# Optimization experiments

Hardware: AMD Instinct MI355X
Metric: run time of the kernel (lower is better)

Reference implementation:

```python
import jax, jax.numpy as jnp
import numpy as np

R = 32
LORA_ALPHA = 64
SCALING = LORA_ALPHA / R  # 2.0
TOPK = 2
NOISE_EPS = 0.01


def setup_inputs() -> dict:
    key = jax.random.key(0)
    ks = jax.random.split(key, 7)
    B, S, D, OUT, E = 4, 2048, 4096, 4096, 8
    x = jax.random.normal(ks[0], (B, S, D), dtype=jnp.float32)
    eof_index = jax.random.randint(ks[1], (B,), 0, S)
    noise = jax.random.normal(ks[2], (B, E), dtype=jnp.float32)
    # learned params (random instead of the zero-init in reset_parameters so the
    # output is non-trivial); Linear weight layout is [out_features, in_features]
    A_w = jax.random.normal(ks[3], (R, D), dtype=jnp.float32) * (1.0 / np.sqrt(D))
    B_w = jax.random.normal(ks[4], (E, OUT, R), dtype=jnp.float32) * (1.0 / np.sqrt(R))
    route_w = jax.random.normal(ks[5], (E, D), dtype=jnp.float32) * (1.0 / np.sqrt(D))
    noise_w = jax.random.normal(ks[6], (E, D), dtype=jnp.float32) * (1.0 / np.sqrt(D))
    return {"x": x, "eof_index": eof_index, "noise": noise,
            "A_w": A_w, "B_w": B_w, "route_w": route_w, "noise_w": noise_w}


def reference(x, eof_index, noise, A_w, B_w, route_w, noise_w):
    B = x.shape[0]
    rows = jnp.arange(B)
    # routing input: token at eof_index for each batch row -> [B, D]
    routing_input = x[rows, eof_index]
    # noisy top-k gating (training path: noisy_gating and is_train are True)
    clean_logits = routing_input @ route_w.T                       # [B, E]
    noise_stddev = jax.nn.softplus(routing_input @ noise_w.T) + NOISE_EPS
    logits = clean_logits + noise * noise_stddev                   # [B, E]
    # torch code takes topk+1 then slices to topk; equivalent to top_k(topk)
    top_vals, top_idx = jax.lax.top_k(logits, TOPK)                # [B, K]
    top_gates = jax.nn.softmax(top_vals.astype(jnp.float32), axis=-1).astype(x.dtype)
    gates = jnp.zeros_like(logits).at[rows[:, None], top_idx].set(top_gates)  # [B, E]
    # shared low-rank projection
    shared = jnp.einsum('bsd,rd->bsr', x, A_w)                     # [B, S, r]
    # sum_i gate_i * (shared @ B_i^T), fused as one contraction
    lora_output = jnp.einsum('bsr,eor,be->bso', shared, B_w, gates)  # [B, S, out]
    return lora_output * SCALING
```

## Files before the change

### kernel.cpp

```cpp
#include <hip/hip_runtime.h>
#include <stdint.h>
#include <math.h>

#define B_ 4
#define S_ 2048
#define D_ 4096
#define O_ 4096
#define E_ 8
#define R_ 32
#define SCALING 2.0f
#define NOISE_EPS 0.01f

typedef unsigned short u16;
typedef short s16x8 __attribute__((ext_vector_type(8)));
typedef float f32x4 __attribute__((ext_vector_type(4)));

__device__ __forceinline__ float b2f(u16 u) {
  union { unsigned int i; float f; } v; v.i = ((unsigned int)u) << 16; return v.f;
}
__device__ __forceinline__ u16 f2b(float f) {
  union { unsigned int i; float f; } v; v.f = f;
  unsigned int i = v.i;
  return (u16)((i + 0x7FFFu + ((i >> 16) & 1u)) >> 16);
}
__device__ __forceinline__ void split2(float f, u16* h, u16* l) {
  u16 hi = f2b(f);
  *h = hi;
  *l = f2b(f - b2f(hi));
}

__device__ __forceinline__ float ld(const void* p, size_t i, int bf) {
  return bf ? b2f(((const u16*)p)[i]) : ((const float*)p)[i];
}

__global__ void k_detect(const unsigned int* __restrict__ xw, int* __restrict__ flag) {
  __shared__ int cnt;
  if (threadIdx.x == 0) cnt = 0;
  __syncthreads();
  unsigned int w = xw[threadIdx.x];
  unsigned int e = (w >> 7) & 0xFFu;
  if (e >= 90u && e <= 140u) atomicAdd(&cnt, 1);
  __syncthreads();
  if (threadIdx.x == 0) *flag = (cnt > 48) ? 1 : 0;
}

__global__ __launch_bounds__(256) void k_logits(
    const void* __restrict__ x, const int* __restrict__ eof,
    const void* __restrict__ route_w, const void* __restrict__ noise_w,
    const int* __restrict__ flag, float* __restrict__ wsf) {
  int bf = *flag;
  int be = blockIdx.x;
  int b = be >> 3, e = be & 7;
  size_t xoff = ((size_t)b * S_ + (size_t)eof[b]) * D_;
  size_t woff = (size_t)e * D_;
  float ac = 0.f, an = 0.f;
  for (int d = threadIdx.x; d < D_; d += 256) {
    float xv = ld(x, xoff + d, bf);
    ac += xv * ld(route_w, woff + d, bf);
    an += xv * ld(noise_w, woff + d, bf);
  }
  __shared__ float rc[256], rn[256];
  rc[threadIdx.x] = ac; rn[threadIdx.x] = an;
  __syncthreads();
  for (int s = 128; s > 0; s >>= 1) {
    if (threadIdx.x < (unsigned)s) {
      rc[threadIdx.x] += rc[threadIdx.x + s];
      rn[threadIdx.x] += rn[threadIdx.x + s];
    }
    __syncthreads();
  }
  if (threadIdx.x == 0) { wsf[16 + be] = rc[0]; wsf[48 + be] = rn[0]; }
}

__global__ void k_gates(const void* __restrict__ noise, const int* __restrict__ flag,
                        float* __restrict__ wsf) {
  int bf = *flag;
  int b = threadIdx.x;
  if (b >= B_) return;
  float lg[E_];
  for (int e = 0; e < E_; e++) {
    float c = wsf[16 + b * 8 + e];
    float n = wsf[48 + b * 8 + e];
    float sp = (n > 20.f) ? n : log1pf(expf(n));
    lg[e] = c + ld(noise, b * 8 + e, bf) * (sp + NOISE_EPS);
  }
  int i1 = 0; float v1 = lg[0];
  for (int e = 1; e < E_; e++) if (lg[e] > v1) { v1 = lg[e]; i1 = e; }
  int i2 = -1; float v2 = -3.0e38f;
  for (int e = 0; e < E_; e++) if (e != i1 && lg[e] > v2) { v2 = lg[e]; i2 = e; }
  float t = expf(v2 - v1);
  float g1 = 1.f / (1.f + t);
  float g2 = t / (1.f + t);
  for (int e = 0; e < E_; e++) wsf[80 + b * 8 + e] = 0.f;
  wsf[80 + b * 8 + i1] = g1;
  wsf[80 + b * 8 + i2] = g2;
}

__global__ __launch_bounds__(256) void k_prepA(
    const float* __restrict__ Aw, const int* __restrict__ flag,
    u16* __restrict__ Aph, u16* __restrict__ Apl) {
  if (*flag) return;
  int flat = blockIdx.x * 256 + threadIdx.x;
  int k32idx = flat >> 7;
  int rem = flat & 127;
  int h = rem >> 6;
  int lane = rem & 63;
  int r = h * 16 + (lane & 15);
  int d = k32idx * 32 + (lane >> 4) * 8;
  const float* src = Aw + (size_t)r * D_ + d;
  f32x4 v0 = *(const f32x4*)src;
  f32x4 v1 = *(const f32x4*)(src + 4);
  ushort4 h0, l0, h1, l1;
  split2(v0[0], &h0.x, &l0.x); split2(v0[1], &h0.y, &l0.y);
  split2(v0[2], &h0.z, &l0.z); split2(v0[3], &h0.w, &l0.w);
  split2(v1[0], &h1.x, &l1.x); split2(v1[1], &h1.y, &l1.y);
  split2(v1[2], &h1.z, &l1.z); split2(v1[3], &h1.w, &l1.w);
  *(ushort4*)(Aph + (size_t)flat * 8)     = h0;
  *(ushort4*)(Aph + (size_t)flat * 8 + 4) = h1;
  *(ushort4*)(Apl + (size_t)flat * 8)     = l0;
  *(ushort4*)(Apl + (size_t)flat * 8 + 4) = l1;
}

__global__ __launch_bounds__(256) void k_wc(
    const void* __restrict__ Bw, const int* __restrict__ flag,
    const float* __restrict__ gates, u16* __restrict__ Wph,
    u16* __restrict__ Wpl) {
  int bf = *flag;
  int idx = blockIdx.x * 256 + threadIdx.x;
  int b = idx >> 15;
  int u = idx & 32767;
  int o = u >> 3, rq = u & 7;
  float g[E_];
#pragma unroll
  for (int e = 0; e < E_; e++) g[e] = gates[b * 8 + e];
  f32x4 acc = {0.f, 0.f, 0.f, 0.f};
  if (bf) {
#pragma unroll
    for (int e = 0; e < E_; e++) {
      ushort4 v = ((const ushort4*)Bw)[(size_t)e * 32768 + u];
      acc[0] += g[e] * b2f(v.x);
      acc[1] += g[e] * b2f(v.y);
      acc[2] += g[e] * b2f(v.z);
      acc[3] += g[e] * b2f(v.w);
    }
  } else {
#pragma unroll
    for (int e = 0; e < E_; e++) {
      f32x4 v = ((const f32x4*)Bw)[(size_t)e * 32768 + u];
      acc += g[e] * v;
    }
  }
  acc *= SCALING;
  ushort4 h, l;
  split2(acc[0], &h.x, &l.x); split2(acc[1], &h.y, &l.y);
  split2(acc[2], &h.z, &l.z); split2(acc[3], &h.w, &l.w);
  int ot = o >> 4;
  int lane = ((rq >> 1) * 16) + (o & 15);
  size_t base = (((size_t)b * 256 + ot) * 64 + lane) * 8 + (rq & 1) * 4;
  *(ushort4*)(Wph + base) = h;
  *(ushort4*)(Wpl + base) = l;
}

__global__ __launch_bounds__(256) void k_sharedM(
    const void* __restrict__ xv, const void* __restrict__ Awv,
    const u16* __restrict__ Aph, const u16* __restrict__ Apl,
    const int* __restrict__ flag, u16* __restrict__ sh2h,
    u16* __restrict__ sh2l) {
  __shared__ u16 xh[4096];
  __shared__ u16 xl[4096];
  __shared__ float red[4][512];
  int bf = *flag;
  int t = threadIdx.x;
  int lane = t & 63;
  int wave = t >> 6;
  int m = lane & 15, kg = lane >> 4;
  int row0 = blockIdx.x * 16;
  f32x4 acc0 = {0.f, 0.f, 0.f, 0.f};
  f32x4 acc1 = {0.f, 0.f, 0.f, 0.f};
  if (bf) {
    int kbase = wave * 1024 + kg * 8;
    const u16* xp = (const u16*)xv + (size_t)(row0 + m) * D_ + kbase;
    const u16* a0 = (const u16*)Awv + (size_t)m * D_ + kbase;
    const u16* a1 = (const u16*)Awv + (size_t)(m + 16) * D_ + kbase;
#pragma unroll 4
    for (int k0 = 0; k0 < 1024; k0 += 32) {
      s16x8 a  = *(const s16x8*)(xp + k0);
      s16x8 b0 = *(const s16x8*)(a0 + k0);
      s16x8 b1 = *(const s16x8*)(a1 + k0);
      acc0 = __builtin_amdgcn_mfma_f32_16x16x32_bf16(a, b0, acc0, 0, 0, 0);
      acc1 = __builtin_amdgcn_mfma_f32_16x16x32_bf16(a, b1, acc1, 0, 0, 0);
    }
  } else {
    int srow = t >> 4;
    int sq = t & 15;
    const float* xrow = (const float*)xv + (size_t)(row0 + srow) * D_;
    for (int kc = 0; kc < D_; kc += 256) {
      __syncthreads();
#pragma unroll
      for (int q = 0; q < 4; q++) {
        int colf = (sq + q * 16) * 4;
        f32x4 v = *(const f32x4*)(xrow + kc + colf);
        ushort4 h, l;
        split2(v[0], &h.x, &l.x); split2(v[1], &h.y, &l.y);
        split2(v[2], &h.z, &l.z); split2(v[3], &h.w, &l.w);
        int swz = (srow * 512 + colf * 2) ^ ((srow & 7) << 4);
        *(ushort4*)((char*)xh + swz) = h;
        *(ushort4*)((char*)xl + swz) = l;
      }
      __syncthreads();
#pragma unroll
      for (int p = 0; p < 2; p++) {
        int k32 = (wave * 2 + p) * 32;
        int boff = (m * 512 + (k32 + kg * 8) * 2) ^ ((m & 7) << 4);
        s16x8 ah = *(const s16x8*)((const char*)xh + boff);
        s16x8 al = *(const s16x8*)((const char*)xl + boff);
        size_t k32idx = (size_t)(kc >> 5) + wave * 2 + p;
        const u16* ph = Aph + (k32idx * 2) * 512;
        const u16* pl = Apl + (k32idx * 2) * 512;
        s16x8 bh0 = *(const s16x8*)(ph + (size_t)lane * 8);
        s16x8 bl0 = *(const s16x8*)(pl + (size_t)lane * 8);
        s16x8 bh1 = *(const s16x8*)(ph + 512 + (size_t)lane * 8);
        s16x8 bl1 = *(const s16x8*)(pl + 512 + (size_t)lane * 8);
        acc0 = __builtin_amdgcn_mfma_f32_16x16x32_bf16(ah, bh0, acc0, 0, 0, 0);
        acc0 = __builtin_amdgcn_mfma_f32_16x16x32_bf16(ah, bl0, acc0, 0, 0, 0);
        acc0 = __builtin_amdgcn_mfma_f32_16x16x32_bf16(al, bh0, acc0, 0, 0, 0);
        acc1 = __builtin_amdgcn_mfma_f32_16x16x32_bf16(ah, bh1, acc1, 0, 0, 0);
        acc1 = __builtin_amdgcn_mfma_f32_16x16x32_bf16(ah, bl1, acc1, 0, 0, 0);
        acc1 = __builtin_amdgcn_mfma_f32_16x16x32_bf16(al, bh1, acc1, 0, 0, 0);
      }
    }
    __syncthreads();
  }
  int crow = (lane >> 4) * 4, ccol = lane & 15;
#pragma unroll
  for (int j = 0; j < 4; j++) {
    red[wave][(crow + j) * 32 + ccol]      = acc0[j];
    red[wave][(crow + j) * 32 + ccol + 16] = acc1[j];
  }
  __syncthreads();
#pragma unroll
  for (int q = 0; q < 2; q++) {
    int e = t + q * 256;
    float s = red[0][e] + red[1][e] + red[2][e] + red[3][e];
    u16 h, l;
    split2(s, &h, &l);
    int row = e >> 5, r = e & 31;
    size_t dst = (size_t)blockIdx.x * 512 + ((size_t)(r >> 3) * 16 + row) * 8 + (r & 7);
    sh2h[dst] = h;
    sh2l[dst] = l;
  }
}

#define OCH 512
__global__ __launch_bounds__(256) void k_outM(
    const u16* __restrict__ sh2h, const u16* __restrict__ sh2l,
    const u16* __restrict__ Wph, const u16* __restrict__ Wpl,
    const int* __restrict__ flag, void* __restrict__ out) {
  __shared__ float C[16][516];
  int bf = *flag;
  int t = threadIdx.x;
  int lane = t & 63, wave = t >> 6;
  int row0 = blockIdx.x * 16;
  int b = row0 >> 11;
  int m = lane & 15;
  s16x8 Ah = *(const s16x8*)(sh2h + (size_t)blockIdx.x * 512 + (size_t)lane * 8);
  s16x8 Al = *(const s16x8*)(sh2l + (size_t)blockIdx.x * 512 + (size_t)lane * 8);
  int crow = (lane >> 4) * 4;
  const u16* whB = Wph + (size_t)b * 131072;
  const u16* wlB = Wpl + (size_t)b * 131072;
  for (int oc = 0; oc < O_; oc += OCH) {
#pragma unroll
    for (int i = 0; i < 8; i++) {
      int otc = wave * 8 + i;
      size_t otg = (size_t)((oc >> 4) + otc);
      s16x8 Bh = *(const s16x8*)(whB + otg * 512 + (size_t)lane * 8);
      s16x8 Bl = *(const s16x8*)(wlB + otg * 512 + (size_t)lane * 8);
      f32x4 acc = {0.f, 0.f, 0.f, 0.f};
      acc = __builtin_amdgcn_mfma_f32_16x16x32_bf16(Ah, Bh, acc, 0, 0, 0);
      acc = __builtin_amdgcn_mfma_f32_16x16x32_bf16(Ah, Bl, acc, 0, 0, 0);
      acc = __builtin_amdgcn_mfma_f32_16x16x32_bf16(Al, Bh, acc, 0, 0, 0);
      int ocol = otc * 16 + m;
#pragma unroll
      for (int j = 0; j < 4; j++) C[crow + j][ocol] = acc[j];
    }
    __syncthreads();
#pragma unroll
    for (int it = 0; it < 8; it++) {
      int row = it * 2 + (t >> 7);
      int col = (t & 127) * 4;
      f32x4 v = *(const f32x4*)&C[row][col];
      size_t off = (size_t)(row0 + row) * O_ + oc + col;
      if (bf) {
        ushort4 o4;
        o4.x = f2b(v[0]); o4.y = f2b(v[1]); o4.z = f2b(v[2]); o4.w = f2b(v[3]);
        *(ushort4*)((u16*)out + off) = o4;
      } else {
        *(f32x4*)((float*)out + off) = v;
      }
    }
    __syncthreads();
  }
}

extern "C" void kernel_launch(void* const* d_in, const int* in_sizes, int n_in,
                              void* d_out, int out_size, void* d_ws, size_t ws_size,
                              hipStream_t stream) {
  const void* x       = d_in[0];
  const int*  eof     = (const int*)d_in[1];
  const void* noise   = d_in[2];
  const void* Aw      = d_in[3];
  const void* Bw      = d_in[4];
  const void* route_w = d_in[5];
  const void* noise_w = d_in[6];
  float* wsf = (float*)d_ws;
  int* flag = (int*)wsf;
  float* gates = wsf + 80;
  u16* Wph  = (u16*)(wsf + 112);
  u16* Wpl  = Wph + (size_t)B_ * O_ * R_;
  u16* Aph  = Wpl + (size_t)B_ * O_ * R_;
  u16* Apl  = Aph + (size_t)R_ * D_;
  u16* sh2h = Apl + (size_t)R_ * D_;
  u16* sh2l = sh2h + (size_t)B_ * S_ * R_;

  k_detect<<<1, 64, 0, stream>>>((const unsigned int*)x, flag);
  k_logits<<<B_ * E_, 256, 0, stream>>>(x, eof, route_w, noise_w, flag, wsf);
  k_gates<<<1, 64, 0, stream>>>(noise, flag, wsf);
  k_prepA<<<64, 256, 0, stream>>>((const float*)Aw, flag, Aph, Apl);
  k_wc<<<(B_ * O_ * R_ / 4) / 256, 256, 0, stream>>>(Bw, flag, gates, Wph, Wpl);
  k_sharedM<<<(B_ * S_) / 16, 256, 0, stream>>>(x, Aw, Aph, Apl, flag, sh2h, sh2l);
  k_outM<<<(B_ * S_) / 16, 256, 0, stream>>>(sh2h, sh2l, Wph, Wpl, flag, d_out);
}
```

Baseline: 315.1 us.

## Fuse shared projection and output GEMM into one kernel, merge prep kernels

Merges the A-weight split and the gated B-weight combine into a single prep launch that picks its role by block index. Fuses the shared low-rank projection and the output GEMM into one kernel: the 16x32 intermediate stays in LDS instead of going to global memory, and the x staging buffer and output staging buffer share a union. This removes two launches and a global round trip for the intermediate, at the cost of higher LDS use per block and a larger fused kernel that may lower occupancy.

```diff
diff --git a/kernel.cpp b/kernel.cpp
--- a/kernel.cpp
+++ b/kernel.cpp
@@ -96,85 +96,90 @@
   wsf[80 + b * 8 + i2] = g2;
 }
 
-__global__ __launch_bounds__(256) void k_prepA(
-    const float* __restrict__ Aw, const int* __restrict__ flag,
+__global__ __launch_bounds__(256) void k_prep(
+    const void* __restrict__ Bw, const float* __restrict__ Aw,
+    const int* __restrict__ flag, const float* __restrict__ gates,
+    u16* __restrict__ Wph, u16* __restrict__ Wpl,
     u16* __restrict__ Aph, u16* __restrict__ Apl) {
-  if (*flag) return;
-  int flat = blockIdx.x * 256 + threadIdx.x;
-  int k32idx = flat >> 7;
-  int rem = flat & 127;
-  int h = rem >> 6;
-  int lane = rem & 63;
-  int r = h * 16 + (lane & 15);
-  int d = k32idx * 32 + (lane >> 4) * 8;
-  const float* src = Aw + (size_t)r * D_ + d;
-  f32x4 v0 = *(const f32x4*)src;
-  f32x4 v1 = *(const f32x4*)(src + 4);
-  ushort4 h0, l0, h1, l1;
-  split2(v0[0], &h0.x, &l0.x); split2(v0[1], &h0.y, &l0.y);
-  split2(v0[2], &h0.z, &l0.z); split2(v0[3], &h0.w, &l0.w);
-  split2(v1[0], &h1.x, &l1.x); split2(v1[1], &h1.y, &l1.y);
-  split2(v1[2], &h1.z, &l1.z); split2(v1[3], &h1.w, &l1.w);
-  *(ushort4*)(Aph + (size_t)flat * 8)     = h0;
-  *(ushort4*)(Aph + (size_t)flat * 8 + 4) = h1;
-  *(ushort4*)(Apl + (size_t)flat * 8)     = l0;
-  *(ushort4*)(Apl + (size_t)flat * 8 + 4) = l1;
-}
-
-__global__ __launch_bounds__(256) void k_wc(
-    const void* __restrict__ Bw, const int* __restrict__ flag,
-    const float* __restrict__ gates, u16* __restrict__ Wph,
-    u16* __restrict__ Wpl) {
   int bf = *flag;
-  int idx = blockIdx.x * 256 + threadIdx.x;
-  int b = idx >> 15;
-  int u = idx & 32767;
-  int o = u >> 3, rq = u & 7;
-  float g[E_];
-#pragma unroll
-  for (int e = 0; e < E_; e++) g[e] = gates[b * 8 + e];
-  f32x4 acc = {0.f, 0.f, 0.f, 0.f};
-  if (bf) {
-#pragma unroll
-    for (int e = 0; e < E_; e++) {
-      ushort4 v = ((const ushort4*)Bw)[(size_t)e * 32768 + u];
-      acc[0] += g[e] * b2f(v.x);
-      acc[1] += g[e] * b2f(v.y);
-      acc[2] += g[e] * b2f(v.z);
-      acc[3] += g[e] * b2f(v.w);
-    }
+  int blk = blockIdx.x;
+  if (blk < 512) {
+    int idx = blk * 256 + threadIdx.x;
+    int b = idx >> 15;
+    int u = idx & 32767;
+    int o = u >> 3, rq = u & 7;
+    float g[E_];
+#pragma unroll
+    for (int e = 0; e < E_; e++) g[e] = gates[b * 8 + e];
+    f32x4 acc = {0.f, 0.f, 0.f, 0.f};
+    if (bf) {
+#pragma unroll
+      for (int e = 0; e < E_; e++) {
+        ushort4 v = ((const ushort4*)Bw)[(size_t)e * 32768 + u];
+        acc[0] += g[e] * b2f(v.x);
+        acc[1] += g[e] * b2f(v.y);
+        acc[2] += g[e] * b2f(v.z);
+        acc[3] += g[e] * b2f(v.w);
+      }
+    } else {
+#pragma unroll
+      for (int e = 0; e < E_; e++) {
+        f32x4 v = ((const f32x4*)Bw)[(size_t)e * 32768 + u];
+        acc += g[e] * v;
+      }
+    }
+    acc *= SCALING;
+    ushort4 h, l;
+    split2(acc[0], &h.x, &l.x); split2(acc[1], &h.y, &l.y);
+    split2(acc[2], &h.z, &l.z); split2(acc[3], &h.w, &l.w);
+    int ot = o >> 4;
+    int lane = ((rq >> 1) * 16) + (o & 15);
+    size_t base = (((size_t)b * 256 + ot) * 64 + lane) * 8 + (rq & 1) * 4;
+    *(ushort4*)(Wph + base) = h;
+    *(ushort4*)(Wpl + base) = l;
   } else {
-#pragma unroll
-    for (int e = 0; e < E_; e++) {
-      f32x4 v = ((const f32x4*)Bw)[(size_t)e * 32768 + u];
-      acc += g[e] * v;
-    }
-  }
-  acc *= SCALING;
-  ushort4 h, l;
-  split2(acc[0], &h.x, &l.x); split2(acc[1], &h.y, &l.y);
-  split2(acc[2], &h.z, &l.z); split2(acc[3], &h.w, &l.w);
-  int ot = o >> 4;
-  int lane = ((rq >> 1) * 16) + (o & 15);
-  size_t base = (((size_t)b * 256 + ot) * 64 + lane) * 8 + (rq & 1) * 4;
-  *(ushort4*)(Wph + base) = h;
-  *(ushort4*)(Wpl + base) = l;
-}
-
-__global__ __launch_bounds__(256) void k_sharedM(
+    if (bf) return;
+    int flat = (blk - 512) * 256 + threadIdx.x;
+    int k32idx = flat >> 7;
+    int rem = flat & 127;
+    int hf = rem >> 6;
+    int lane = rem & 63;
+    int r = hf * 16 + (lane & 15);
+    int d = k32idx * 32 + (lane >> 4) * 8;
+    const float* src = Aw + (size_t)r * D_ + d;
+    f32x4 v0 = *(const f32x4*)src;
+    f32x4 v1 = *(const f32x4*)(src + 4);
+    ushort4 h0, l0, h1, l1;
+    split2(v0[0], &h0.x, &l0.x); split2(v0[1], &h0.y, &l0.y);
+    split2(v0[2], &h0.z, &l0.z); split2(v0[3], &h0.w, &l0.w);
+    split2(v1[0], &h1.x, &l1.x); split2(v1[1], &h1.y, &l1.y);
+    split2(v1[2], &h1.z, &l1.z); split2(v1[3], &h1.w, &l1.w);
+    *(ushort4*)(Aph + (size_t)flat * 8)     = h0;
+    *(ushort4*)(Aph + (size_t)flat * 8 + 4) = h1;
+    *(ushort4*)(Apl + (size_t)flat * 8)     = l0;
+    *(ushort4*)(Apl + (size_t)flat * 8 + 4) = l1;
+  }
+}
+
+#define OCH 512
+__global__ __launch_bounds__(256) void k_mega(
     const void* __restrict__ xv, const void* __restrict__ Awv,
     const u16* __restrict__ Aph, const u16* __restrict__ Apl,
-    const int* __restrict__ flag, u16* __restrict__ sh2h,
-    u16* __restrict__ sh2l) {
-  __shared__ u16 xh[4096];
-  __shared__ u16 xl[4096];
-  __shared__ float red[4][512];
+    const u16* __restrict__ Wph, const u16* __restrict__ Wpl,
+    const int* __restrict__ flag, void* __restrict__ out) {
+  __shared__ union SM {
+    struct { u16 xh[4096]; u16 xl[4096]; float red[4][512]; } p1;
+    float C[16][516];
+  } sm;
+  __shared__ u16 shAh[512], shAl[512];
   int bf = *flag;
   int t = threadIdx.x;
   int lane = t & 63;
   int wave = t >> 6;
   int m = lane & 15, kg = lane >> 4;
   int row0 = blockIdx.x * 16;
+  int b = row0 >> 11;
+
   f32x4 acc0 = {0.f, 0.f, 0.f, 0.f};
   f32x4 acc1 = {0.f, 0.f, 0.f, 0.f};
   if (bf) {
@@ -204,16 +209,16 @@
         split2(v[0], &h.x, &l.x); split2(v[1], &h.y, &l.y);
         split2(v[2], &h.z, &l.z); split2(v[3], &h.w, &l.w);
         int swz = (srow * 512 + colf * 2) ^ ((srow & 7) << 4);
-        *(ushort4*)((char*)xh + swz) = h;
-        *(ushort4*)((char*)xl + swz) = l;
+        *(ushort4*)((char*)sm.p1.xh + swz) = h;
+        *(ushort4*)((char*)sm.p1.xl + swz) = l;
       }
       __syncthreads();
 #pragma unroll
       for (int p = 0; p < 2; p++) {
         int k32 = (wave * 2 + p) * 32;
         int boff = (m * 512 + (k32 + kg * 8) * 2) ^ ((m & 7) << 4);
-        s16x8 ah = *(const s16x8*)((const char*)xh + boff);
-        s16x8 al = *(const s16x8*)((const char*)xl + boff);
+        s16x8 ah = *(const s16x8*)((const char*)sm.p1.xh + boff);
+        s16x8 al = *(const s16x8*)((const char*)sm.p1.xl + boff);
         size_t k32idx = (size_t)(kc >> 5) + wave * 2 + p;
         const u16* ph = Aph + (k32idx * 2) * 512;
         const u16* pl = Apl + (k32idx * 2) * 512;
@@ -229,46 +234,34 @@
         acc1 = __builtin_amdgcn_mfma_f32_16x16x32_bf16(al, bh1, acc1, 0, 0, 0);
       }
     }
-    __syncthreads();
-  }
+  }
+  __syncthreads();
   int crow = (lane >> 4) * 4, ccol = lane & 15;
 #pragma unroll
   for (int j = 0; j < 4; j++) {
-    red[wave][(crow + j) * 32 + ccol]      = acc0[j];
-    red[wave][(crow + j) * 32 + ccol + 16] = acc1[j];
+    sm.p1.red[wave][(crow + j) * 32 + ccol]      = acc0[j];
+    sm.p1.red[wave][(crow + j) * 32 + ccol + 16] = acc1[j];
   }
   __syncthreads();
 #pragma unroll
   for (int q = 0; q < 2; q++) {
     int e = t + q * 256;
-    float s = red[0][e] + red[1][e] + red[2][e] + red[3][e];
+    float s = sm.p1.red[0][e] + sm.p1.red[1][e] + sm.p1.red[2][e] + sm.p1.red[3][e];
     u16 h, l;
     split2(s, &h, &l);
     int row = e >> 5, r = e & 31;
-    size_t dst = (size_t)blockIdx.x * 512 + ((size_t)(r >> 3) * 16 + row) * 8 + (r & 7);
-    sh2h[dst] = h;
-    sh2l[dst] = l;
-  }
-}
-
-#define OCH 512
-__global__ __launch_bounds__(256) void k_outM(
-    const u16* __restrict__ sh2h, const u16* __restrict__ sh2l,
-    const u16* __restrict__ Wph, const u16* __restrict__ Wpl,
-    const int* __restrict__ flag, void* __restrict__ out) {
-  __shared__ float C[16][516];
-  int bf = *flag;
-  int t = threadIdx.x;
-  int lane = t & 63, wave = t >> 6;
-  int row0 = blockIdx.x * 16;
-  int b = row0 >> 11;
-  int m = lane & 15;
-  s16x8 Ah = *(const s16x8*)(sh2h + (size_t)blockIdx.x * 512 + (size_t)lane * 8);
-  s16x8 Al = *(const s16x8*)(sh2l + (size_t)blockIdx.x * 512 + (size_t)lane * 8);
-  int crow = (lane >> 4) * 4;
+    int dst = ((r >> 3) * 16 + row) * 8 + (r & 7);
+    shAh[dst] = h;
+    shAl[dst] = l;
+  }
+  __syncthreads();
+
+  s16x8 Ah = *(const s16x8*)(shAh + (size_t)lane * 8);
+  s16x8 Al = *(const s16x8*)(shAl + (size_t)lane * 8);
   const u16* whB = Wph + (size_t)b * 131072;
   const u16* wlB = Wpl + (size_t)b * 131072;
   for (int oc = 0; oc < O_; oc += OCH) {
+    __syncthreads();
 #pragma unroll
     for (int i = 0; i < 8; i++) {
       int otc = wave * 8 + i;
@@ -281,14 +274,14 @@
       acc = __builtin_amdgcn_mfma_f32_16x16x32_bf16(Al, Bh, acc, 0, 0, 0);
       int ocol = otc * 16 + m;
 #pragma unroll
-      for (int j = 0; j < 4; j++) C[crow + j][ocol] = acc[j];
+      for (int j = 0; j < 4; j++) sm.C[crow + j][ocol] = acc[j];
     }
     __syncthreads();
 #pragma unroll
     for (int it = 0; it < 8; it++) {
       int row = it * 2 + (t >> 7);
       int col = (t & 127) * 4;
-      f32x4 v = *(const f32x4*)&C[row][col];
+      f32x4 v = *(const f32x4*)&sm.C[row][col];
       size_t off = (size_t)(row0 + row) * O_ + oc + col;
       if (bf) {
         ushort4 o4;
@@ -298,7 +291,6 @@
         *(f32x4*)((float*)out + off) = v;
       }
     }
-    __syncthreads();
   }
 }
 
@@ -319,14 +311,12 @@
   u16* Wpl  = Wph + (size_t)B_ * O_ * R_;
   u16* Aph  = Wpl + (size_t)B_ * O_ * R_;
   u16* Apl  = Aph + (size_t)R_ * D_;
-  u16* sh2h = Apl + (size_t)R_ * D_;
-  u16* sh2l = sh2h + (size_t)B_ * S_ * R_;
 
   k_detect<<<1, 64, 0, stream>>>((const unsigned int*)x, flag);
   k_logits<<<B_ * E_, 256, 0, stream>>>(x, eof, route_w, noise_w, flag, wsf);
   k_gates<<<1, 64, 0, stream>>>(noise, flag, wsf);
-  k_prepA<<<64, 256, 0, stream>>>((const float*)Aw, flag, Aph, Apl);
-  k_wc<<<(B_ * O_ * R_ / 4) / 256, 256, 0, stream>>>(Bw, flag, gates, Wph, Wpl);
-  k_sharedM<<<(B_ * S_) / 16, 256, 0, stream>>>(x, Aw, Aph, Apl, flag, sh2h, sh2l);
-  k_outM<<<(B_ * S_) / 16, 256, 0, stream>>>(sh2h, sh2l, Wph, Wpl, flag, d_out);
-}
+  k_prep<<<512 + 64, 256, 0, stream>>>(Bw, (const float*)Aw, flag, gates,
+                                       Wph, Wpl, Aph, Apl);
+  k_mega<<<(B_ * S_) / 16, 256, 0, stream>>>(x, Aw, Aph, Apl, Wph, Wpl,
+                                             flag, d_out);
+}
```

Result: faster. 303.6 us (-3.7%).
